# Performance work log

Hardware: AMD Instinct MI355X
Metric: run time of the kernel (lower is better)

The kernel has to match this reference:

```python
import jax, jax.numpy as jnp
import numpy as np

V = 50000   # input_size == output_size (one-hot vocab)
H = 256     # hidden_size
B = 512     # batch_size
L = 1       # num_layers

def setup_inputs() -> dict:
    key = jax.random.key(0)
    ks = jax.random.split(key, 9)
    s = 1.0 / np.sqrt(H)  # torch default uniform(-1/sqrt(H), 1/sqrt(H))
    inp = {
        "input": jax.random.randint(ks[0], (B,), 0, V, dtype=jnp.int64 if jax.config.jax_enable_x64 else jnp.int32),
        "target": jax.random.randint(ks[1], (B,), 0, V, dtype=jnp.int64 if jax.config.jax_enable_x64 else jnp.int32),
        "hidden": jax.random.normal(ks[2], (L, B, H), dtype=jnp.float32),
        "w_ih": jax.random.uniform(ks[3], (3 * H, V), jnp.float32, -s, s),
        "w_hh": jax.random.uniform(ks[4], (3 * H, H), jnp.float32, -s, s),
        "b_ih": jax.random.uniform(ks[5], (3 * H,), jnp.float32, -s, s),
        "b_hh": jax.random.uniform(ks[6], (3 * H,), jnp.float32, -s, s),
        "w_out": jax.random.uniform(ks[7], (V, H), jnp.float32, -s, s),
        "b_out": jax.random.uniform(ks[8], (V,), jnp.float32, -s, s),
    }
    return inp

def reference(input, target, hidden, w_ih, w_hh, b_ih, b_hh, w_out, b_out):
    # one-hot(input) @ w_ih.T is exactly a row-gather from w_ih.T  -> (B, 3H)
    h0 = hidden[0]                              # (B, H), num_layers == 1
    x_proj = w_ih.T[input] + b_ih               # (B, 3H)
    h_proj = h0 @ w_hh.T + b_hh                 # (B, 3H)
    xr, xz, xn = jnp.split(x_proj, 3, axis=-1)
    hr, hz, hn = jnp.split(h_proj, 3, axis=-1)
    r = jax.nn.sigmoid(xr + hr)                 # reset gate
    z = jax.nn.sigmoid(xz + hz)                 # update gate
    n = jnp.tanh(xn + r * hn)                   # candidate
    h1 = (1.0 - z) * n + z * h0                 # (B, H)
    logit = jnp.tanh(h1 @ w_out.T + b_out)      # (B, V)
    return logit, h1[None]                      # (B,V), (1,B,H)
```

## Files before the change

kernel.cpp:

```cpp
#include <hip/hip_runtime.h>
#include <hip/hip_bf16.h>

#define VOCAB 50000
#define HID   256
#define BATCH 512
#define GH    768

typedef __attribute__((ext_vector_type(8))) __bf16 bf16x8;
typedef __attribute__((ext_vector_type(4))) float f32x4;
typedef __attribute__((ext_vector_type(4))) unsigned int u32x4;

union BFrag {
    bf16x8 v;
    u32x4  q;
    __bf16 b[8];
};

__device__ __forceinline__ float fast_sigmoid(float x) {
    return 1.0f / (1.0f + __expf(-x));
}
__device__ __forceinline__ float fast_tanh(float x) {
    return 1.0f - 2.0f / (1.0f + __expf(2.0f * x));
}

__device__ __forceinline__ void cvt8(BFrag& t, f32x4 lo, f32x4 hi) {
    t.b[0] = (__bf16)lo.x; t.b[1] = (__bf16)lo.y;
    t.b[2] = (__bf16)lo.z; t.b[3] = (__bf16)lo.w;
    t.b[4] = (__bf16)hi.x; t.b[5] = (__bf16)hi.y;
    t.b[6] = (__bf16)hi.z; t.b[7] = (__bf16)hi.w;
}

template <int EPI, int ASRC>
__global__ __launch_bounds__(256, 4) void gemm_col(
    const void* __restrict__ Asrc, const float* __restrict__ Bm,
    float* __restrict__ C, const float* __restrict__ bias,
    int Ncols, int mChunks)
{
    __shared__ char ldsA[64 * 512];

    const int tid  = threadIdx.x;
    const int wid  = tid >> 6;
    const int lane = tid & 63;
    const int r    = lane & 15;
    const int g    = lane >> 4;
    const int col  = blockIdx.x * 64 + wid * 16 + r;
    const int bcol = col < Ncols ? col : (Ncols - 1);

    BFrag bf[8];
    {
        const f32x4* wrow = reinterpret_cast<const f32x4*>(Bm + (size_t)bcol * 256);
        #pragma unroll
        for (int kk = 0; kk < 8; kk++)
            cvt8(bf[kk], wrow[kk * 8 + g * 2], wrow[kk * 8 + g * 2 + 1]);
    }
    float biasv = 0.0f;
    if (EPI == 1) biasv = bias[bcol];

    u32x4 areg[8];
    auto load_chunk = [&](int c) {
        const int mbase = (blockIdx.y * mChunks + c) * 64;
        if (ASRC == 1) {
            const u32x4* src = reinterpret_cast<const u32x4*>(
                (const unsigned short*)Asrc + (size_t)mbase * 256);
            #pragma unroll
            for (int i = 0; i < 8; i++) areg[i] = src[tid + i * 256];
        } else {
            const f32x4* src = reinterpret_cast<const f32x4*>(
                (const float*)Asrc + (size_t)mbase * 256);
            #pragma unroll
            for (int i = 0; i < 8; i++) {
                int u = tid + i * 256;
                BFrag t; cvt8(t, src[2 * u], src[2 * u + 1]);
                areg[i] = t.q;
            }
        }
    };
    auto write_lds = [&]() {
        #pragma unroll
        for (int i = 0; i < 8; i++) {
            int u = tid + i * 256;
            int row = u >> 5, j = u & 31;
            int byte = row * 512 + ((j ^ (row & 7)) << 4);
            *reinterpret_cast<u32x4*>(&ldsA[byte]) = areg[i];
        }
    };

    load_chunk(0);

    for (int c = 0; c < mChunks; c++) {
        if (c > 0)
            asm volatile("s_barrier" ::: "memory");

        write_lds();
        asm volatile("s_waitcnt lgkmcnt(0)\n\ts_barrier" ::: "memory");

        if (c + 1 < mChunks) load_chunk(c + 1);

        f32x4 acc[4];
        #pragma unroll
        for (int m = 0; m < 4; m++) acc[m] = (f32x4){0.f, 0.f, 0.f, 0.f};

        #pragma unroll
        for (int kk = 0; kk < 8; kk++) {
            #pragma unroll
            for (int m = 0; m < 4; m++) {
                int arow = m * 16 + r;
                int byte = arow * 512 + (((kk * 4 + g) ^ (arow & 7)) << 4);
                BFrag a;
                a.q = *reinterpret_cast<const u32x4*>(&ldsA[byte]);
                acc[m] = __builtin_amdgcn_mfma_f32_16x16x32_bf16(a.v, bf[kk].v, acc[m], 0, 0, 0);
            }
        }

        if (col < Ncols) {
            const int rowbase = (blockIdx.y * mChunks + c) * 64;
            #pragma unroll
            for (int m = 0; m < 4; m++) {
                #pragma unroll
                for (int j = 0; j < 4; j++) {
                    float v = acc[m][j];
                    if (EPI == 1) v = fast_tanh(v + biasv);
                    C[(size_t)(rowbase + m * 16 + g * 4 + j) * Ncols + col] = v;
                }
            }
        }
    }
}

__global__ __launch_bounds__(256) void gru_gate(
    const int* __restrict__ inp, const float* __restrict__ hidden,
    const float* __restrict__ w_ih, const float* __restrict__ b_ih,
    const float* __restrict__ b_hh, const float* __restrict__ hproj,
    float* __restrict__ h1out, unsigned short* __restrict__ h1bf)
{
    const int b = blockIdx.x;
    const int k = threadIdx.x;
    const int c = inp[b];

    float xr = w_ih[(size_t)k * VOCAB + c]         + b_ih[k];
    float xz = w_ih[(size_t)(k + 256) * VOCAB + c] + b_ih[k + 256];
    float xn = w_ih[(size_t)(k + 512) * VOCAB + c] + b_ih[k + 512];

    float hr = hproj[b * GH + k]       + b_hh[k];
    float hz = hproj[b * GH + 256 + k] + b_hh[k + 256];
    float hn = hproj[b * GH + 512 + k] + b_hh[k + 512];

    float rg = fast_sigmoid(xr + hr);
    float zg = fast_sigmoid(xz + hz);
    float ng = fast_tanh(xn + rg * hn);
    float h0 = hidden[b * HID + k];
    float h1 = (1.0f - zg) * ng + zg * h0;

    h1out[b * HID + k] = h1;
    __bf16 hb = (__bf16)h1;
    h1bf[b * HID + k] = __builtin_bit_cast(unsigned short, hb);
}

extern "C" void kernel_launch(void* const* d_in, const int* in_sizes, int n_in,
                              void* d_out, int out_size, void* d_ws, size_t ws_size,
                              hipStream_t stream) {
    const int*   input  = (const int*)  d_in[0];
    const float* hidden = (const float*)d_in[2];
    const float* w_ih   = (const float*)d_in[3];
    const float* w_hh   = (const float*)d_in[4];
    const float* b_ih   = (const float*)d_in[5];
    const float* b_hh   = (const float*)d_in[6];
    const float* w_out  = (const float*)d_in[7];
    const float* b_out  = (const float*)d_in[8];

    float* logit = (float*)d_out;
    float* h1    = (float*)d_out + (size_t)BATCH * VOCAB;

    float*          hproj = (float*)d_ws;
    unsigned short* h1bf  = (unsigned short*)((char*)d_ws + (size_t)BATCH * GH * 4);

    dim3 g1(GH / 64, BATCH / 64);
    gemm_col<0, 0><<<g1, 256, 0, stream>>>(hidden, w_hh, hproj, nullptr, GH, 1);

    gru_gate<<<BATCH, 256, 0, stream>>>(input, hidden, w_ih, b_ih, b_hh, hproj,
                                        h1, h1bf);

    dim3 g3((VOCAB + 63) / 64, 1);
    gemm_col<1, 1><<<g3, 256, 0, stream>>>(h1bf, w_out, logit, b_out, VOCAB, 8);
}
```

Measured before the change: 61.19 us.

## Double-buffer LDS A-tiles in GEMM with smaller row chunks and nontemporal weight loads

Splits the LDS A tile into two 32-row buffers so the next chunk is written to LDS while MFMAs run on the current one, with one barrier per chunk instead of two. Chunks shrink from 64 to 32 rows, so the output GEMM loops 16 times and the hidden-projection grid doubles in the batch direction. The w_out column weights, read only once, are loaded with nontemporal hints to avoid polluting cache. In exchange each chunk issues fewer MFMAs and there are more loop iterations and stores of smaller granularity.

```diff
diff --git a/kernel.cpp b/kernel.cpp
--- a/kernel.cpp
+++ b/kernel.cpp
@@ -30,13 +30,13 @@
     t.b[6] = (__bf16)hi.z; t.b[7] = (__bf16)hi.w;
 }
 
-template <int EPI, int ASRC>
-__global__ __launch_bounds__(256, 4) void gemm_col(
+template <int EPI, int ASRC, int NTB>
+__global__ __launch_bounds__(256, 4) void gemm_db(
     const void* __restrict__ Asrc, const float* __restrict__ Bm,
     float* __restrict__ C, const float* __restrict__ bias,
     int Ncols, int mChunks)
 {
-    __shared__ char ldsA[64 * 512];
+    __shared__ char ldsA[2][32 * 512];
 
     const int tid  = threadIdx.x;
     const int wid  = tid >> 6;
@@ -50,80 +50,96 @@
     {
         const f32x4* wrow = reinterpret_cast<const f32x4*>(Bm + (size_t)bcol * 256);
         #pragma unroll
-        for (int kk = 0; kk < 8; kk++)
-            cvt8(bf[kk], wrow[kk * 8 + g * 2], wrow[kk * 8 + g * 2 + 1]);
+        for (int kk = 0; kk < 8; kk++) {
+            f32x4 lo, hi;
+            if (NTB) {
+                lo = __builtin_nontemporal_load(&wrow[kk * 8 + g * 2]);
+                hi = __builtin_nontemporal_load(&wrow[kk * 8 + g * 2 + 1]);
+            } else {
+                lo = wrow[kk * 8 + g * 2];
+                hi = wrow[kk * 8 + g * 2 + 1];
+            }
+            cvt8(bf[kk], lo, hi);
+        }
     }
+    #pragma unroll
+    for (int kk = 0; kk < 8; kk++)
+        asm volatile("" : "+v"(bf[kk].q));
     float biasv = 0.0f;
     if (EPI == 1) biasv = bias[bcol];
 
-    u32x4 areg[8];
+    u32x4 areg[4];
     auto load_chunk = [&](int c) {
-        const int mbase = (blockIdx.y * mChunks + c) * 64;
+        const int mbase = (blockIdx.y * mChunks + c) * 32;
         if (ASRC == 1) {
             const u32x4* src = reinterpret_cast<const u32x4*>(
                 (const unsigned short*)Asrc + (size_t)mbase * 256);
             #pragma unroll
-            for (int i = 0; i < 8; i++) areg[i] = src[tid + i * 256];
+            for (int i = 0; i < 4; i++) areg[i] = src[tid + i * 256];
         } else {
             const f32x4* src = reinterpret_cast<const f32x4*>(
                 (const float*)Asrc + (size_t)mbase * 256);
             #pragma unroll
-            for (int i = 0; i < 8; i++) {
+            for (int i = 0; i < 4; i++) {
                 int u = tid + i * 256;
                 BFrag t; cvt8(t, src[2 * u], src[2 * u + 1]);
                 areg[i] = t.q;
             }
         }
     };
-    auto write_lds = [&]() {
+    auto write_lds = [&](int buf) {
         #pragma unroll
-        for (int i = 0; i < 8; i++) {
+        for (int i = 0; i < 4; i++) {
             int u = tid + i * 256;
             int row = u >> 5, j = u & 31;
             int byte = row * 512 + ((j ^ (row & 7)) << 4);
-            *reinterpret_cast<u32x4*>(&ldsA[byte]) = areg[i];
+            *reinterpret_cast<u32x4*>(&ldsA[buf][byte]) = areg[i];
         }
     };
 
     load_chunk(0);
+    write_lds(0);
+    if (mChunks > 1) load_chunk(1);
+    asm volatile("s_waitcnt lgkmcnt(0)\n\ts_barrier" ::: "memory");
 
     for (int c = 0; c < mChunks; c++) {
-        if (c > 0)
-            asm volatile("s_barrier" ::: "memory");
-
-        write_lds();
-        asm volatile("s_waitcnt lgkmcnt(0)\n\ts_barrier" ::: "memory");
-
-        if (c + 1 < mChunks) load_chunk(c + 1);
-
-        f32x4 acc[4];
-        #pragma unroll
-        for (int m = 0; m < 4; m++) acc[m] = (f32x4){0.f, 0.f, 0.f, 0.f};
+        const int cur = c & 1;
+        if (c + 1 < mChunks) {
+            write_lds(cur ^ 1);
+            if (c + 2 < mChunks) load_chunk(c + 2);
+        }
+
+        f32x4 acc[2];
+        acc[0] = (f32x4){0.f, 0.f, 0.f, 0.f};
+        acc[1] = (f32x4){0.f, 0.f, 0.f, 0.f};
 
         #pragma unroll
         for (int kk = 0; kk < 8; kk++) {
             #pragma unroll
-            for (int m = 0; m < 4; m++) {
+            for (int m = 0; m < 2; m++) {
                 int arow = m * 16 + r;
                 int byte = arow * 512 + (((kk * 4 + g) ^ (arow & 7)) << 4);
                 BFrag a;
-                a.q = *reinterpret_cast<const u32x4*>(&ldsA[byte]);
+                a.q = *reinterpret_cast<const u32x4*>(&ldsA[cur][byte]);
                 acc[m] = __builtin_amdgcn_mfma_f32_16x16x32_bf16(a.v, bf[kk].v, acc[m], 0, 0, 0);
             }
         }
 
         if (col < Ncols) {
-            const int rowbase = (blockIdx.y * mChunks + c) * 64;
-            #pragma unroll
-            for (int m = 0; m < 4; m++) {
+            const int rowbase = (blockIdx.y * mChunks + c) * 32 + g * 4;
+            #pragma unroll
+            for (int m = 0; m < 2; m++) {
                 #pragma unroll
                 for (int j = 0; j < 4; j++) {
                     float v = acc[m][j];
                     if (EPI == 1) v = fast_tanh(v + biasv);
-                    C[(size_t)(rowbase + m * 16 + g * 4 + j) * Ncols + col] = v;
+                    C[(size_t)(rowbase + m * 16 + j) * Ncols + col] = v;
                 }
             }
         }
+
+        if (c + 1 < mChunks)
+            asm volatile("s_waitcnt lgkmcnt(0)\n\ts_barrier" ::: "memory");
     }
 }
 
@@ -174,12 +190,12 @@
     float*          hproj = (float*)d_ws;
     unsigned short* h1bf  = (unsigned short*)((char*)d_ws + (size_t)BATCH * GH * 4);
 
-    dim3 g1(GH / 64, BATCH / 64);
-    gemm_col<0, 0><<<g1, 256, 0, stream>>>(hidden, w_hh, hproj, nullptr, GH, 1);
+    dim3 g1(GH / 64, BATCH / 32);
+    gemm_db<0, 0, 0><<<g1, 256, 0, stream>>>(hidden, w_hh, hproj, nullptr, GH, 1);
 
     gru_gate<<<BATCH, 256, 0, stream>>>(input, hidden, w_ih, b_ih, b_hh, hproj,
                                         h1, h1bf);
 
     dim3 g3((VOCAB + 63) / 64, 1);
-    gemm_col<1, 1><<<g3, 256, 0, stream>>>(h1bf, w_out, logit, b_out, VOCAB, 8);
-}
+    gemm_db<1, 1, 1><<<g3, 256, 0, stream>>>(h1bf, w_out, logit, b_out, VOCAB, 16);
+}
```

Result: slower. 69.42 us (+13.4%).
